# Performance work log

Hardware: AMD Instinct MI355X
Metric: run time of the kernel (lower is better)

## Reference

```python
import jax, jax.numpy as jnp
import numpy as np

N_LBL, E_LBL, K = 32, 16, 16          # node labels, edge labels, tensor_neurons
DN, DE = 2 * N_LBL, 2 * E_LBL         # TNM input dims
REG = [16, 8, 4]                      # reg_neurons
N = M = 6000


def setup_inputs() -> dict:
    key = jax.random.key(0)
    ks = jax.random.split(key, 24)
    u = lambda k, s: jax.random.uniform(k, s, dtype=jnp.float32)
    g = lambda k, s: jax.random.normal(k, s, dtype=jnp.float32) * 0.1
    inp = dict(
        emb1=u(ks[0], (N, N_LBL)), emb2=u(ks[1], (N, N_LBL)),
        adj1=u(ks[2], (N, N)), adj2=u(ks[3], (N, N)),
        edge_attr1=u(ks[4], (M, E_LBL)), edge_attr2=u(ks[5], (M, E_LBL)),
        edge_adj1=u(ks[6], (M, M)), edge_adj2=u(ks[7], (M, M)),
        avg_v=jnp.float32(50.0),
        # tensor networks: nc, in, ie share D=DN (stacked on axis 0); ec uses DE
        Wn=g(ks[8], (3, DN, DN, K)), Wbn=g(ks[9], (3, K, 2 * DN)), bn=g(ks[10], (3, K)),
        We=g(ks[11], (DE, DE, K)), Wbe=g(ks[12], (K, 2 * DE)), be=g(ks[13], (K,)),
        # 4 MLP stacks (order nc, in, ie, ec), torch Linear layout [out, in]
        mlp1_w=g(ks[14], (4, REG[0], K)), mlp1_b=g(ks[15], (4, REG[0])),
        mlp2_w=g(ks[16], (4, REG[1], REG[0])), mlp2_b=g(ks[17], (4, REG[1])),
        mlp3_w=g(ks[18], (4, REG[2], REG[1])), mlp3_b=g(ks[19], (4, REG[2])),
        score_w=g(ks[20], (4, REG[2])), score_b=g(ks[21], (4,)),
    )
    return inp


def _tnm(e1, e2, W, Wb, b):
    # SimGNN-style bilinear tensor network on pooled vectors e1,e2: [D]
    scoring = jnp.einsum('d,dek,e->k', e1, W, e2)
    block = Wb @ jnp.concatenate([e1, e2])
    return jax.nn.relu(scoring + block + b)  # [K]


def reference(emb1, emb2, adj1, adj2, edge_attr1, edge_attr2, edge_adj1, edge_adj2,
              avg_v, Wn, Wbn, bn, We, Wbe, be,
              mlp1_w, mlp1_b, mlp2_w, mlp2_b, mlp3_w, mlp3_b, score_w, score_b):
    def gal_pass(adj, feat):
        h1 = adj @ feat          # GraphAggregationLayer: mm(adj, input)
        h2 = adj @ h1
        return h1, h2

    g1h1, g1h2 = gal_pass(adj1, emb1)
    g2h1, g2h2 = gal_pass(adj2, emb2)
    e1h1, _ = gal_pass(edge_adj1, edge_attr1)
    e2h1, _ = gal_pass(edge_adj2, edge_attr2)

    # concat + sum-pool -> single vectors of width 2D
    g1_01 = jnp.concatenate([emb1, g1h1], axis=1).sum(0)   # [DN]
    g2_01 = jnp.concatenate([emb2, g2h1], axis=1).sum(0)
    g1_12 = jnp.concatenate([g1h1, g1h2], axis=1).sum(0)
    g2_12 = jnp.concatenate([g2h1, g2h2], axis=1).sum(0)
    e1_01 = jnp.concatenate([edge_attr1, e1h1], axis=1).sum(0)  # [DE]
    e2_01 = jnp.concatenate([edge_attr2, e2h1], axis=1).sum(0)

    # node branches nc, in (use 01 pooled) and ie (uses 12 pooled)
    e1s = jnp.stack([g1_01, g1_01, g1_12])
    e2s = jnp.stack([g2_01, g2_01, g2_12])
    s_node = jax.vmap(_tnm)(e1s, e2s, Wn, Wbn, bn)          # [3, K]
    s_ec = _tnm(e1_01, e2_01, We, Wbe, be)                  # [K]
    s = jnp.concatenate([s_node, s_ec[None]], axis=0)       # [4, K] (nc,in,ie,ec)

    h = jax.nn.relu(jnp.einsum('boi,bi->bo', mlp1_w, s) + mlp1_b)
    h = jax.nn.relu(jnp.einsum('boi,bi->bo', mlp2_w, h) + mlp2_b)
    h = jax.nn.relu(jnp.einsum('boi,bi->bo', mlp3_w, h) + mlp3_b)
    scores4 = jax.nn.sigmoid(jnp.einsum('bi,bi->b', score_w, h) + score_b)  # [4]

    # final order: nc, in, ec, ie
    score = scores4[jnp.array([0, 1, 3, 2])]
    pre_ged = jnp.sum(-jnp.log(score) * avg_v)              # target_mode == 'exp'
    pre_sim = jnp.exp(-pre_ged / avg_v)
    return pre_sim, pre_ged, score
```

## Files before the change

kernel.cpp:

```cpp
#include <hip/hip_runtime.h>
#include <cstdint>
#include <cmath>

#define THREADS 256
#define ROWS_PER_BLK 64
#define LDP 6016

template <bool WEIGHTED>
__global__ void colsum2_kernel(const float* __restrict__ A0,
                               const float* __restrict__ A1,
                               const float* __restrict__ w0,
                               const float* __restrict__ w1,
                               float* __restrict__ P,
                               int N, int nParts) {
    const float* A = blockIdx.z ? A1 : A0;
    const float* w = blockIdx.z ? w1 : w0;
    float* Pm = P + (size_t)blockIdx.z * nParts * LDP;

    int col = blockIdx.x * (THREADS * 4) + threadIdx.x * 4;
    if (col >= N) return;
    int r0 = blockIdx.y * ROWS_PER_BLK;
    int r1 = r0 + ROWS_PER_BLK;
    if (r1 > N) r1 = N;
    float ax = 0.f, ay = 0.f, az = 0.f, aw = 0.f;
    const float* p = A + (size_t)r0 * N + col;
#pragma unroll 4
    for (int r = r0; r < r1; ++r, p += N) {
        float4 v = *reinterpret_cast<const float4*>(p);
        float wr = WEIGHTED ? w[r] : 1.0f;
        ax += wr * v.x;
        ay += wr * v.y;
        az += wr * v.z;
        aw += wr * v.w;
    }
    float4 o = {ax, ay, az, aw};
    *reinterpret_cast<float4*>(&Pm[(size_t)blockIdx.y * LDP + col]) = o;
}

__global__ void reduce2_kernel(const float* __restrict__ P,
                               float* __restrict__ out0,
                               float* __restrict__ out1,
                               int N, int nParts) {
    int col = blockIdx.x * THREADS + threadIdx.x;
    if (col >= N) return;
    const float* p = P + (size_t)blockIdx.y * nParts * LDP + col;
    float* out = blockIdx.y ? out1 : out0;
    float s = 0.f;
#pragma unroll 4
    for (int i = 0; i < nParts; ++i, p += LDP) s += *p;
    out[col] = s;
}

__global__ void feat_all_kernel(const float* __restrict__ emb1,
                                const float* __restrict__ emb2,
                                const float* __restrict__ eat1,
                                const float* __restrict__ eat2,
                                const float* __restrict__ c1,
                                const float* __restrict__ d1,
                                const float* __restrict__ c2,
                                const float* __restrict__ d2,
                                const float* __restrict__ ce1,
                                const float* __restrict__ ce2,
                                float* __restrict__ n1,
                                float* __restrict__ n2,
                                float* __restrict__ eg1,
                                float* __restrict__ eg2,
                                int Nn, int Ne) {
    int unit = blockIdx.y;
    const float *feat, *c, *d;
    float* out;
    int total, log2L;
    bool hasQ;
    if (unit == 0)      { feat = emb1; c = c1;  d = d1;      out = n1;  total = Nn * 32; log2L = 5; hasQ = true;  }
    else if (unit == 1) { feat = emb2; c = c2;  d = d2;      out = n2;  total = Nn * 32; log2L = 5; hasQ = true;  }
    else if (unit == 2) { feat = eat1; c = ce1; d = nullptr; out = eg1; total = Ne * 16; log2L = 4; hasQ = false; }
    else                { feat = eat2; c = ce2; d = nullptr; out = eg2; total = Ne * 16; log2L = 4; hasQ = false; }

    int stride = gridDim.x * blockDim.x;
    int idx = blockIdx.x * blockDim.x + threadIdx.x;
    int L = 1 << log2L;
    int l = idx & (L - 1);
    float as = 0.f, ap = 0.f, aq = 0.f;
    for (int i = idx; i < total; i += stride) {
        float v = feat[i];
        int r = i >> log2L;
        as += v;
        ap += c[r] * v;
        if (hasQ) aq += d[r] * v;
    }
    atomicAdd(&out[l], as);
    atomicAdd(&out[L + l], ap);
    if (hasQ) atomicAdd(&out[2 * L + l], aq);
}

__global__ void scoring_kernel(const float* __restrict__ Wn,
                               const float* __restrict__ We,
                               const float* __restrict__ n1,
                               const float* __restrict__ n2,
                               const float* __restrict__ eg1,
                               const float* __restrict__ eg2,
                               float* __restrict__ scoring) {
    int b = blockIdx.y;
    int chunk = blockIdx.x;
    const float *W, *e1, *e2;
    int total, log2D;
    if (b < 3) {
        W = Wn + (size_t)b * (64 * 64 * 16);
        e1 = n1 + (b == 2 ? 32 : 0);
        e2 = n2 + (b == 2 ? 32 : 0);
        total = 64 * 64 * 16;
        log2D = 6;
    } else {
        W = We;
        e1 = eg1;
        e2 = eg2;
        total = 32 * 32 * 16;
        log2D = 5;
    }
    int begin = chunk * 4096 + threadIdx.x;
    int end = (chunk + 1) * 4096;
    if (end > total) end = total;
    float acc = 0.f;
    for (int idx = begin; idx < end; idx += 256) {
        int de = idx >> 4;
        int e = de & ((1 << log2D) - 1);
        int dd = de >> log2D;
        acc += e1[dd] * e2[e] * W[idx];
    }
    __shared__ float red[256];
    red[threadIdx.x] = acc;
    __syncthreads();
    if (threadIdx.x < 16) {
        float s = 0.f;
        for (int t = threadIdx.x; t < 256; t += 16) s += red[t];
        atomicAdd(&scoring[b * 16 + threadIdx.x], s);
    }
}

__global__ void final_kernel(const float* __restrict__ scoring,
                             const float* __restrict__ n1,
                             const float* __restrict__ n2,
                             const float* __restrict__ eg1,
                             const float* __restrict__ eg2,
                             const float* __restrict__ Wbn,
                             const float* __restrict__ bn,
                             const float* __restrict__ Wbe,
                             const float* __restrict__ be,
                             const float* __restrict__ m1w,
                             const float* __restrict__ m1b,
                             const float* __restrict__ m2w,
                             const float* __restrict__ m2b,
                             const float* __restrict__ m3w,
                             const float* __restrict__ m3b,
                             const float* __restrict__ sw,
                             const float* __restrict__ sb,
                             const float* __restrict__ avg_v,
                             float* __restrict__ out) {
    __shared__ float sval[4][16];
    __shared__ float scores[4];
    int t = threadIdx.x;
    int b = t >> 4, k = t & 15;

    float blk;
    if (b < 3) {
        const float* e1 = n1 + (b == 2 ? 32 : 0);
        const float* e2 = n2 + (b == 2 ? 32 : 0);
        const float* wb = Wbn + (size_t)b * (16 * 128) + k * 128;
        float s = 0.f;
        for (int j = 0; j < 64; ++j) s += wb[j] * e1[j];
        for (int j = 0; j < 64; ++j) s += wb[64 + j] * e2[j];
        blk = s + bn[b * 16 + k];
    } else {
        const float* wb = Wbe + k * 64;
        float s = 0.f;
        for (int j = 0; j < 32; ++j) s += wb[j] * eg1[j];
        for (int j = 0; j < 32; ++j) s += wb[32 + j] * eg2[j];
        blk = s + be[k];
    }
    float v = scoring[b * 16 + k] + blk;
    sval[b][k] = v > 0.f ? v : 0.f;
    __syncthreads();

    if (t < 4) {
        float h1[16], h2[8], h3[4];
        for (int o = 0; o < 16; ++o) {
            float a = m1b[t * 16 + o];
            for (int i = 0; i < 16; ++i) a += m1w[(t * 16 + o) * 16 + i] * sval[t][i];
            h1[o] = a > 0.f ? a : 0.f;
        }
        for (int o = 0; o < 8; ++o) {
            float a = m2b[t * 8 + o];
            for (int i = 0; i < 16; ++i) a += m2w[(t * 8 + o) * 16 + i] * h1[i];
            h2[o] = a > 0.f ? a : 0.f;
        }
        for (int o = 0; o < 4; ++o) {
            float a = m3b[t * 4 + o];
            for (int i = 0; i < 8; ++i) a += m3w[(t * 4 + o) * 8 + i] * h2[i];
            h3[o] = a > 0.f ? a : 0.f;
        }
        float z = sb[t];
        for (int i = 0; i < 4; ++i) z += sw[t * 4 + i] * h3[i];
        scores[t] = 1.0f / (1.0f + expf(-z));
    }
    __syncthreads();

    if (t == 0) {
        const int ord[4] = {0, 1, 3, 2};
        float av = avg_v[0];
        float acc = 0.f;
        for (int j = 0; j < 4; ++j) {
            float sc = scores[ord[j]];
            out[2 + j] = sc;
            acc += -logf(sc);
        }
        float ged = acc * av;
        out[1] = ged;
        out[0] = expf(-ged / av);
    }
}

extern "C" void kernel_launch(void* const* d_in, const int* in_sizes, int n_in,
                              void* d_out, int out_size, void* d_ws, size_t ws_size,
                              hipStream_t stream) {
    const float* emb1  = (const float*)d_in[0];
    const float* emb2  = (const float*)d_in[1];
    const float* adj1  = (const float*)d_in[2];
    const float* adj2  = (const float*)d_in[3];
    const float* eat1  = (const float*)d_in[4];
    const float* eat2  = (const float*)d_in[5];
    const float* eadj1 = (const float*)d_in[6];
    const float* eadj2 = (const float*)d_in[7];
    const float* avg_v = (const float*)d_in[8];
    const float* Wn    = (const float*)d_in[9];
    const float* Wbn   = (const float*)d_in[10];
    const float* bn    = (const float*)d_in[11];
    const float* We    = (const float*)d_in[12];
    const float* Wbe   = (const float*)d_in[13];
    const float* be    = (const float*)d_in[14];
    const float* m1w   = (const float*)d_in[15];
    const float* m1b   = (const float*)d_in[16];
    const float* m2w   = (const float*)d_in[17];
    const float* m2b   = (const float*)d_in[18];
    const float* m3w   = (const float*)d_in[19];
    const float* m3b   = (const float*)d_in[20];
    const float* sw    = (const float*)d_in[21];
    const float* sb    = (const float*)d_in[22];

    int Nn = in_sizes[0] / 32;
    int Ne = in_sizes[4] / 16;
    int nPartsN = (Nn + ROWS_PER_BLK - 1) / ROWS_PER_BLK;
    int nPartsE = (Ne + ROWS_PER_BLK - 1) / ROWS_PER_BLK;
    int nPartsMax = nPartsN > nPartsE ? nPartsN : nPartsE;

    float* ws  = (float*)d_ws;
    float* P   = ws;
    float* c1  = P + (size_t)2 * nPartsMax * LDP;
    float* d1  = c1 + Nn;
    float* c2  = d1 + Nn;
    float* d2  = c2 + Nn;
    float* ce1 = d2 + Nn;
    float* ce2 = ce1 + Ne;
    float* n1  = ce2 + Ne;
    float* n2  = n1 + 96;
    float* eg1 = n2 + 96;
    float* eg2 = eg1 + 32;
    float* scoring = eg2 + 32;
    hipMemsetAsync(n1, 0, 320 * sizeof(float), stream);

    dim3 blk(THREADS);
    dim3 gridN((Nn + THREADS * 4 - 1) / (THREADS * 4), nPartsN, 2);
    dim3 gridE((Ne + THREADS * 4 - 1) / (THREADS * 4), nPartsE, 2);
    dim3 gridRN((Nn + THREADS - 1) / THREADS, 2);
    dim3 gridRE((Ne + THREADS - 1) / THREADS, 2);

    colsum2_kernel<false><<<gridN, blk, 0, stream>>>(adj1, adj2, nullptr, nullptr, P, Nn, nPartsN);
    reduce2_kernel<<<gridRN, blk, 0, stream>>>(P, c1, c2, Nn, nPartsN);
    colsum2_kernel<true ><<<gridN, blk, 0, stream>>>(adj1, adj2, c1, c2, P, Nn, nPartsN);
    reduce2_kernel<<<gridRN, blk, 0, stream>>>(P, d1, d2, Nn, nPartsN);
    colsum2_kernel<false><<<gridE, blk, 0, stream>>>(eadj1, eadj2, nullptr, nullptr, P, Ne, nPartsE);
    reduce2_kernel<<<gridRE, blk, 0, stream>>>(P, ce1, ce2, Ne, nPartsE);

    feat_all_kernel<<<dim3(16, 4), blk, 0, stream>>>(emb1, emb2, eat1, eat2,
                                                     c1, d1, c2, d2, ce1, ce2,
                                                     n1, n2, eg1, eg2, Nn, Ne);

    scoring_kernel<<<dim3(16, 4), blk, 0, stream>>>(Wn, We, n1, n2, eg1, eg2, scoring);

    final_kernel<<<1, 64, 0, stream>>>(scoring, n1, n2, eg1, eg2,
                                       Wbn, bn, Wbe, be,
                                       m1w, m1b, m2w, m2b, m3w, m3b, sw, sb,
                                       avg_v, (float*)d_out);
}
```

Before: 256.6 us.

## Switch column-sum to row-slab blocks with full-width rows and atomic reduction

Each block now owns a slab of about 12 consecutive rows and sweeps the full row width with six float4 chunks per thread, instead of a 64-row by 1024-column tile. The partial reduction is split across 8 row groups with float4 loads and atomicAdd into pre-zeroed outputs. The aim is long contiguous row reads and more parallelism in the reduce. In exchange it uses a larger partial buffer (about 500 slabs), adds more partial-sum traffic and atomics, and assumes the edge matrices are the same size as the node matrices.

```diff
diff --git a/kernel.cpp b/kernel.cpp
--- a/kernel.cpp
+++ b/kernel.cpp
@@ -3,52 +3,90 @@
 #include <cmath>
 
 #define THREADS 256
-#define ROWS_PER_BLK 64
 #define LDP 6016
+#define MAXCHUNK 6
+#define RGROUPS 8
 
 template <bool WEIGHTED>
-__global__ void colsum2_kernel(const float* __restrict__ A0,
-                               const float* __restrict__ A1,
-                               const float* __restrict__ w0,
-                               const float* __restrict__ w1,
-                               float* __restrict__ P,
-                               int N, int nParts) {
-    const float* A = blockIdx.z ? A1 : A0;
-    const float* w = blockIdx.z ? w1 : w0;
-    float* Pm = P + (size_t)blockIdx.z * nParts * LDP;
-
+__global__ void colsum_slab_kernel(const float* __restrict__ A0,
+                                   const float* __restrict__ A1,
+                                   const float* __restrict__ w0,
+                                   const float* __restrict__ w1,
+                                   float* __restrict__ P,
+                                   int N, int nSlabs, int R) {
+    const int z = blockIdx.y;
+    const float* __restrict__ A = z ? A1 : A0;
+    const float* __restrict__ w = z ? w1 : w0;
+    float* Pm = P + (size_t)z * nSlabs * LDP;
+
+    const int slab = blockIdx.x;
+    int r0 = slab * R;
+    int r1 = r0 + R;
+    if (r1 > N) r1 = N;
+    const int col0 = threadIdx.x * 4;
+
+    float4 acc[MAXCHUNK];
+#pragma unroll
+    for (int c = 0; c < MAXCHUNK; ++c) acc[c] = float4{0.f, 0.f, 0.f, 0.f};
+
+    const float* row = A + (size_t)r0 * N;
+    for (int r = r0; r < r1; ++r, row += N) {
+        float wr = WEIGHTED ? w[r] : 1.0f;
+        float4 v[MAXCHUNK];
+#pragma unroll
+        for (int c = 0; c < MAXCHUNK; ++c) {
+            int col = c * 1024 + col0;
+            if (col < N) v[c] = *reinterpret_cast<const float4*>(row + col);
+        }
+#pragma unroll
+        for (int c = 0; c < MAXCHUNK; ++c) {
+            int col = c * 1024 + col0;
+            if (col < N) {
+                acc[c].x += wr * v[c].x;
+                acc[c].y += wr * v[c].y;
+                acc[c].z += wr * v[c].z;
+                acc[c].w += wr * v[c].w;
+            }
+        }
+    }
+#pragma unroll
+    for (int c = 0; c < MAXCHUNK; ++c) {
+        int col = c * 1024 + col0;
+        if (col < N)
+            *reinterpret_cast<float4*>(&Pm[(size_t)slab * LDP + col]) = acc[c];
+    }
+}
+
+__global__ void reduce_atomic_kernel(const float* __restrict__ P,
+                                     float* __restrict__ out0,
+                                     float* __restrict__ out1,
+                                     int N, int nSlabs) {
     int col = blockIdx.x * (THREADS * 4) + threadIdx.x * 4;
     if (col >= N) return;
-    int r0 = blockIdx.y * ROWS_PER_BLK;
-    int r1 = r0 + ROWS_PER_BLK;
-    if (r1 > N) r1 = N;
-    float ax = 0.f, ay = 0.f, az = 0.f, aw = 0.f;
-    const float* p = A + (size_t)r0 * N + col;
-#pragma unroll 4
-    for (int r = r0; r < r1; ++r, p += N) {
-        float4 v = *reinterpret_cast<const float4*>(p);
-        float wr = WEIGHTED ? w[r] : 1.0f;
-        ax += wr * v.x;
-        ay += wr * v.y;
-        az += wr * v.z;
-        aw += wr * v.w;
-    }
-    float4 o = {ax, ay, az, aw};
-    *reinterpret_cast<float4*>(&Pm[(size_t)blockIdx.y * LDP + col]) = o;
-}
-
-__global__ void reduce2_kernel(const float* __restrict__ P,
-                               float* __restrict__ out0,
-                               float* __restrict__ out1,
-                               int N, int nParts) {
-    int col = blockIdx.x * THREADS + threadIdx.x;
-    if (col >= N) return;
-    const float* p = P + (size_t)blockIdx.y * nParts * LDP + col;
-    float* out = blockIdx.y ? out1 : out0;
-    float s = 0.f;
-#pragma unroll 4
-    for (int i = 0; i < nParts; ++i, p += LDP) s += *p;
-    out[col] = s;
+    int z = blockIdx.y;
+    int chunk = (nSlabs + RGROUPS - 1) / RGROUPS;
+    int i0 = blockIdx.z * chunk;
+    int i1 = i0 + chunk;
+    if (i1 > nSlabs) i1 = nSlabs;
+    float* out = z ? out1 : out0;
+
+    const float* p = P + (size_t)z * nSlabs * LDP + (size_t)i0 * LDP + col;
+    float4 s0 = {0, 0, 0, 0}, s1 = {0, 0, 0, 0};
+    int i = i0;
+    for (; i + 2 <= i1; i += 2, p += 2 * LDP) {
+        float4 a = *reinterpret_cast<const float4*>(p);
+        float4 b = *reinterpret_cast<const float4*>(p + LDP);
+        s0.x += a.x; s0.y += a.y; s0.z += a.z; s0.w += a.w;
+        s1.x += b.x; s1.y += b.y; s1.z += b.z; s1.w += b.w;
+    }
+    if (i < i1) {
+        float4 a = *reinterpret_cast<const float4*>(p);
+        s0.x += a.x; s0.y += a.y; s0.z += a.z; s0.w += a.w;
+    }
+    atomicAdd(&out[col + 0], s0.x + s1.x);
+    atomicAdd(&out[col + 1], s0.y + s1.y);
+    atomicAdd(&out[col + 2], s0.z + s1.z);
+    atomicAdd(&out[col + 3], s0.w + s1.w);
 }
 
 __global__ void feat_all_kernel(const float* __restrict__ emb1,
@@ -248,37 +286,42 @@
 
     int Nn = in_sizes[0] / 32;
     int Ne = in_sizes[4] / 16;
-    int nPartsN = (Nn + ROWS_PER_BLK - 1) / ROWS_PER_BLK;
-    int nPartsE = (Ne + ROWS_PER_BLK - 1) / ROWS_PER_BLK;
-    int nPartsMax = nPartsN > nPartsE ? nPartsN : nPartsE;
+    int N = Nn;
+
+    size_t availF = ws_size / 4;
+    size_t reserveF = 8 * (size_t)N + 4096;
+    size_t perMat = (availF > reserveF) ? (availF - reserveF) / 2 : 0;
+    int maxSlabs = (int)(perMat / LDP);
+    int nSlabs = (N + 11) / 12;
+    if (nSlabs > maxSlabs) nSlabs = maxSlabs > 0 ? maxSlabs : 1;
+    int R = (N + nSlabs - 1) / nSlabs;
+    nSlabs = (N + R - 1) / R;
 
     float* ws  = (float*)d_ws;
     float* P   = ws;
-    float* c1  = P + (size_t)2 * nPartsMax * LDP;
-    float* d1  = c1 + Nn;
-    float* c2  = d1 + Nn;
-    float* d2  = c2 + Nn;
-    float* ce1 = d2 + Nn;
-    float* ce2 = ce1 + Ne;
-    float* n1  = ce2 + Ne;
+    float* c1  = P + (size_t)2 * nSlabs * LDP;
+    float* d1  = c1 + N;
+    float* c2  = d1 + N;
+    float* d2  = c2 + N;
+    float* ce1 = d2 + N;
+    float* ce2 = ce1 + N;
+    float* n1  = ce2 + N;
     float* n2  = n1 + 96;
     float* eg1 = n2 + 96;
     float* eg2 = eg1 + 32;
     float* scoring = eg2 + 32;
-    hipMemsetAsync(n1, 0, 320 * sizeof(float), stream);
+    hipMemsetAsync(c1, 0, (6 * (size_t)N + 320) * sizeof(float), stream);
 
     dim3 blk(THREADS);
-    dim3 gridN((Nn + THREADS * 4 - 1) / (THREADS * 4), nPartsN, 2);
-    dim3 gridE((Ne + THREADS * 4 - 1) / (THREADS * 4), nPartsE, 2);
-    dim3 gridRN((Nn + THREADS - 1) / THREADS, 2);
-    dim3 gridRE((Ne + THREADS - 1) / THREADS, 2);
-
-    colsum2_kernel<false><<<gridN, blk, 0, stream>>>(adj1, adj2, nullptr, nullptr, P, Nn, nPartsN);
-    reduce2_kernel<<<gridRN, blk, 0, stream>>>(P, c1, c2, Nn, nPartsN);
-    colsum2_kernel<true ><<<gridN, blk, 0, stream>>>(adj1, adj2, c1, c2, P, Nn, nPartsN);
-    reduce2_kernel<<<gridRN, blk, 0, stream>>>(P, d1, d2, Nn, nPartsN);
-    colsum2_kernel<false><<<gridE, blk, 0, stream>>>(eadj1, eadj2, nullptr, nullptr, P, Ne, nPartsE);
-    reduce2_kernel<<<gridRE, blk, 0, stream>>>(P, ce1, ce2, Ne, nPartsE);
+    dim3 gridS(nSlabs, 2);
+    dim3 gridR((N + THREADS * 4 - 1) / (THREADS * 4), 2, RGROUPS);
+
+    colsum_slab_kernel<false><<<gridS, blk, 0, stream>>>(adj1, adj2, nullptr, nullptr, P, N, nSlabs, R);
+    reduce_atomic_kernel<<<gridR, blk, 0, stream>>>(P, c1, c2, N, nSlabs);
+    colsum_slab_kernel<true ><<<gridS, blk, 0, stream>>>(adj1, adj2, c1, c2, P, N, nSlabs, R);
+    reduce_atomic_kernel<<<gridR, blk, 0, stream>>>(P, d1, d2, N, nSlabs);
+    colsum_slab_kernel<false><<<gridS, blk, 0, stream>>>(eadj1, eadj2, nullptr, nullptr, P, N, nSlabs, R);
+    reduce_atomic_kernel<<<gridR, blk, 0, stream>>>(P, ce1, ce2, N, nSlabs);
 
     feat_all_kernel<<<dim3(16, 4), blk, 0, stream>>>(emb1, emb2, eat1, eat2,
                                                      c1, d1, c2, d2, ce1, ce2,
```

Measured after the change: 274.5 us. 7.0% more time.
